# Performance work log

Hardware: AMD Instinct MI355X
Metric: run time of the kernel (lower is better)

Reference implementation:

```python
import jax, jax.numpy as jnp
import numpy as np

B, N, FEAT = 4, 100000, 11
NUM_SP = 512  # superpoints per sample
H1, H2, H3, E = 128, 256, 512, 384


def setup_inputs() -> dict:
    key = jax.random.key(0)
    ks = jax.random.split(key, 10)
    s = 0.02
    return {
        "full_features": jax.random.normal(ks[0], (B, N, FEAT), dtype=jnp.float32),
        "full_super_indices": jax.random.randint(ks[1], (B, N), 0, NUM_SP, dtype=jnp.int32),
        "W1": jax.random.normal(ks[2], (H1, FEAT), dtype=jnp.float32) * s,
        "b1": jnp.zeros((H1,), jnp.float32),
        "W2": jax.random.normal(ks[3], (H2, H1), dtype=jnp.float32) * s,
        "b2": jnp.zeros((H2,), jnp.float32),
        "W3": jax.random.normal(ks[4], (H3, H3), dtype=jnp.float32) * s,
        "b3": jnp.zeros((H3,), jnp.float32),
        "W4": jax.random.normal(ks[5], (E, H3), dtype=jnp.float32) * s,
        "b4": jnp.zeros((E,), jnp.float32),
    }


def reference(full_features, full_super_indices, W1, b1, W2, b2, W3, b3, W4, b4):
    # Vectorized form of the per-superpoint mini-PointNet:
    # conv1x1 MLP on points, segment-max pool, concat global+local, MLP, segment-max.
    x = full_features.reshape(B * N, FEAT)
    # first_conv: Conv1d(feat,128,1) -> Conv1d(128,256,1), no activation in between
    h = x @ W1.T + b1
    h = h @ W2.T + b2                                   # [B*N, 256]
    # global segment ids (batch-offset superpoint ids)
    seg = (full_super_indices.astype(jnp.int32) + jnp.arange(B, dtype=jnp.int32)[:, None] * NUM_SP).reshape(-1)
    gmax = jax.ops.segment_max(h, seg, num_segments=B * NUM_SP)  # [B*S, 256]
    g = gmax[seg]                                       # broadcast global feature back to points
    feat = jnp.concatenate([g, h], axis=-1)             # [B*N, 512] (global first, as in torch.cat)
    # second_conv: Conv1d(512,512,1) -> ReLU -> Conv1d(512,E,1)
    y = jax.nn.relu(feat @ W3.T + b3)
    y = y @ W4.T + b4                                   # [B*N, E]
    out = jax.ops.segment_max(y, seg, num_segments=B * NUM_SP)
    return out.reshape(B, NUM_SP, E)
```

## Files before the change

kernel.cpp:

```cpp
#include <hip/hip_runtime.h>
#include <hip/hip_bf16.h>
#include <math.h>

#define BB    4
#define NN    100000
#define NFEAT 11
#define NSP   512
#define NSEG  (BB*NSP)
#define NPTS  (BB*NN)
#define H2    256
#define H3    512
#define EE    384
#define MT    64
#define GS    (MT*8)
#define MI_N  (MT/16)
#define MAXL  15
#define RSEG  512
#define MAXS  12
#define ENCNI 0x007FFFFFu

typedef __attribute__((ext_vector_type(8))) short short8;
typedef __attribute__((ext_vector_type(4))) float f32x4;

__device__ __forceinline__ ushort f2bf(float f) {
  unsigned u = __builtin_bit_cast(unsigned, f);
  unsigned r = (u + 0x7FFFu + ((u >> 16) & 1u)) >> 16;
  return (ushort)r;
}
__device__ __forceinline__ unsigned encf(float f) {
  unsigned u = __builtin_bit_cast(unsigned, f);
  return u ^ ((unsigned)((int)u >> 31) | 0x80000000u);
}
__device__ __forceinline__ float decf(unsigned e) {
  unsigned u = (e & 0x80000000u) ? (e ^ 0x80000000u) : ~e;
  return __builtin_bit_cast(float, u);
}

__global__ void init_all(int* __restrict__ counts, int* __restrict__ cursor,
                         unsigned* __restrict__ gmaxEnc, unsigned* __restrict__ out_enc) {
  int i = blockIdx.x * 256 + threadIdx.x;
  if (i < NSEG * EE) out_enc[i] = ENCNI;
  if (i < NSEG * H2) gmaxEnc[i] = ENCNI;
  if (i < NSEG) { counts[i] = 0; cursor[i] = 0; }
}

__global__ void hist_kernel(const int* __restrict__ sidx, int* __restrict__ counts) {
  int i = blockIdx.x * blockDim.x + threadIdx.x;
  if (i < NPTS) {
    int seg = sidx[i] + (i / NN) * NSP;
    atomicAdd(&counts[seg], 1);
  }
}

__global__ void scan_kernel(const int* __restrict__ counts, int* __restrict__ offs) {
  __shared__ int buf[1024];
  int t = threadIdx.x;
  int c0 = counts[2 * t], c1 = counts[2 * t + 1];
  int s = c0 + c1;
  buf[t] = s;
  __syncthreads();
  for (int d = 1; d < 1024; d <<= 1) {
    int add = (t >= d) ? buf[t - d] : 0;
    __syncthreads();
    buf[t] += add;
    __syncthreads();
  }
  int incl = buf[t];
  int excl = incl - s;
  offs[2 * t] = excl;
  offs[2 * t + 1] = excl + c0;
  if (t == 1023) offs[2048] = incl;
}

__global__ void scatter_kernel(const int* __restrict__ sidx, const int* __restrict__ offs,
                               int* __restrict__ cursor, int* __restrict__ perm,
                               int* __restrict__ segp) {
  int i = blockIdx.x * blockDim.x + threadIdx.x;
  if (i < NPTS) {
    int seg = sidx[i] + (i / NN) * NSP;
    int pos = offs[seg] + atomicAdd(&cursor[seg], 1);
    perm[pos] = i;
    segp[pos] = seg;
  }
}

__global__ void prep_weights(const float* __restrict__ W1, const float* __restrict__ b1,
                             const float* __restrict__ W2, const float* __restrict__ b2,
                             const float* __restrict__ W3, const float* __restrict__ W4,
                             float* __restrict__ W12, float* __restrict__ b12,
                             float* __restrict__ W3gT, ushort* __restrict__ W3hP,
                             ushort* __restrict__ W4P) {
  int u = blockIdx.x * blockDim.x + threadIdx.x;
  if (u < H2 * NFEAT) {
    int c = u / NFEAT, f = u - c * NFEAT;
    float acc = 0.f;
    for (int j = 0; j < 128; ++j) acc += W2[c * 128 + j] * W1[j * NFEAT + f];
    W12[u] = acc;
  } else if (u < 3072) {
    int c = u - H2 * NFEAT;
    float acc = b2[c];
    for (int j = 0; j < 128; ++j) acc += W2[c * 128 + j] * b1[j];
    b12[c] = acc;
  } else if (u < 3072 + 131072) {
    int v = u - 3072;
    int c = v >> 9, o = v & 511;
    W3gT[v] = W3[o * H3 + c];
  } else if (u < 134144 + 16384) {
    int v = u - 134144;
    int ks = v >> 11, rem = v & 2047;
    int nt = rem >> 6, l = rem & 63;
    int n = nt * 16 + (l & 15);
    #pragma unroll
    for (int j = 0; j < 8; ++j) {
      int k = ks * 32 + (l >> 4) * 8 + j;
      W3hP[(size_t)v * 8 + j] = f2bf(W3[n * H3 + H2 + k]);
    }
  } else if (u < 150528 + 24576) {
    int v = u - 150528;
    int ks = v / 1536, rem = v - ks * 1536;
    int nt = rem >> 6, l = rem & 63;
    int n = nt * 16 + (l & 15);
    #pragma unroll
    for (int j = 0; j < 8; ++j) {
      int k = ks * 32 + (l >> 4) * 8 + j;
      W4P[(size_t)v * 8 + j] = f2bf(W4[n * H3 + k]);
    }
  }
}

template <bool STOREH>
__global__ __launch_bounds__(512) void gmax_kernel(
    const float* __restrict__ x, const int* __restrict__ perm,
    const int* __restrict__ segp,
    const float* __restrict__ W12, const float* __restrict__ b12,
    unsigned* __restrict__ gmaxEnc, ushort* __restrict__ hG) {
  __shared__ float xs[RSEG * NFEAT];
  __shared__ float W12s[H2 * NFEAT];
  __shared__ float b12s[H2];
  __shared__ int   segd[RSEG];
  __shared__ unsigned gmaxL[MAXS * H2];

  const int t = threadIdx.x;
  const int mbeg = blockIdx.x * RSEG;
  const int nvalid = min(RSEG, NPTS - mbeg);

  for (int u = t; u < RSEG * NFEAT; u += 512) {
    int p = u / NFEAT, f = u - p * NFEAT;
    xs[u] = (p < nvalid) ? x[(size_t)perm[mbeg + p] * NFEAT + f] : 0.f;
  }
  for (int u = t; u < H2 * NFEAT; u += 512) W12s[u] = W12[u];
  if (t < H2) b12s[t] = b12[t];
  segd[t] = (t < nvalid) ? segp[mbeg + t] : segp[mbeg + nvalid - 1];
  for (int u = t; u < MAXS * H2; u += 512) gmaxL[u] = ENCNI;
  __syncthreads();

  const int s_lo = segd[0];
  const int s_hi = segd[nvalid - 1];
  const bool fb = (s_hi - s_lo + 1) > MAXS;

  const int g  = t >> 4;
  const int r0 = t & 15;
  const int cb = g * 8;

  float w12r[8][NFEAT], bbr[8];
  #pragma unroll
  for (int cj = 0; cj < 8; ++cj) {
    bbr[cj] = b12s[cb + cj];
    #pragma unroll
    for (int f = 0; f < NFEAT; ++f) w12r[cj][f] = W12s[(cb + cj) * NFEAT + f];
  }

  float m[8];
  #pragma unroll
  for (int cj = 0; cj < 8; ++cj) m[cj] = -INFINITY;
  int cur = segd[r0];
  bool any = false;

  for (int k = 0; k < 32; ++k) {
    int row = r0 + k * 16;
    if (row >= nvalid) break;
    int sg = segd[row];
    if (sg != cur) {
      #pragma unroll
      for (int cj = 0; cj < 8; ++cj) {
        unsigned e = encf(m[cj]);
        if (fb) atomicMax(&gmaxEnc[(size_t)cur * H2 + cb + cj], e);
        else    atomicMax(&gmaxL[(cur - s_lo) * H2 + cb + cj], e);
      }
      cur = sg;
      #pragma unroll
      for (int cj = 0; cj < 8; ++cj) m[cj] = -INFINITY;
    }
    float acc[8];
    #pragma unroll
    for (int cj = 0; cj < 8; ++cj) acc[cj] = bbr[cj];
    #pragma unroll
    for (int f = 0; f < NFEAT; ++f) {
      float xv = xs[row * NFEAT + f];
      #pragma unroll
      for (int cj = 0; cj < 8; ++cj) acc[cj] += w12r[cj][f] * xv;
    }
    if (STOREH) {
      uint4 pkt;
      pkt.x = (unsigned)f2bf(acc[0]) | ((unsigned)f2bf(acc[1]) << 16);
      pkt.y = (unsigned)f2bf(acc[2]) | ((unsigned)f2bf(acc[3]) << 16);
      pkt.z = (unsigned)f2bf(acc[4]) | ((unsigned)f2bf(acc[5]) << 16);
      pkt.w = (unsigned)f2bf(acc[6]) | ((unsigned)f2bf(acc[7]) << 16);
      int pt = mbeg + row;
      *(uint4*)&hG[(size_t)(pt >> 6) * 16384 + ((size_t)g * 64 + (pt & 63)) * 8] = pkt;
    }
    #pragma unroll
    for (int cj = 0; cj < 8; ++cj) m[cj] = fmaxf(m[cj], acc[cj]);
    any = true;
  }
  if (any) {
    #pragma unroll
    for (int cj = 0; cj < 8; ++cj) {
      unsigned e = encf(m[cj]);
      if (fb) atomicMax(&gmaxEnc[(size_t)cur * H2 + cb + cj], e);
      else    atomicMax(&gmaxL[(cur - s_lo) * H2 + cb + cj], e);
    }
  }

  __syncthreads();
  if (!fb) {
    int nloc = s_hi - s_lo + 1;
    for (int u = t; u < nloc * H2; u += 512) {
      int sg = s_lo + (u >> 8);
      unsigned v = gmaxL[u];
      if (sg > s_lo && sg < s_hi) gmaxEnc[(size_t)sg * H2 + (u & 255)] = v;
      else atomicMax(&gmaxEnc[(size_t)sg * H2 + (u & 255)], v);
    }
  }
}

__global__ __launch_bounds__(256) void gpart_kernel(
    const unsigned* __restrict__ gmaxEnc, const float* __restrict__ W3gT,
    const float* __restrict__ b3, float* __restrict__ gpartG) {
  __shared__ float gm[8 * 256];
  const int t = threadIdx.x;
  const int b = blockIdx.x;
  for (int u = t; u < 8 * 256; u += 256) gm[u] = decf(gmaxEnc[(size_t)b * 8 * 256 + u]);
  __syncthreads();
  const float bb0 = b3[t], bb1 = b3[t + 256];
  float a0[8], a1[8];
  #pragma unroll
  for (int sg = 0; sg < 8; ++sg) { a0[sg] = bb0; a1[sg] = bb1; }
  for (int c = 0; c < 256; ++c) {
    float w0 = W3gT[c * 512 + t], w1 = W3gT[c * 512 + t + 256];
    #pragma unroll
    for (int sg = 0; sg < 8; ++sg) {
      float gv = gm[sg * 256 + c];
      a0[sg] += w0 * gv; a1[sg] += w1 * gv;
    }
  }
  #pragma unroll
  for (int sg = 0; sg < 8; ++sg) {
    size_t s = (size_t)b * 8 + sg;
    gpartG[s * 512 + t] = a0[sg];
    gpartG[s * 512 + t + 256] = a1[sg];
  }
}

__global__ void finalize_kernel(const unsigned* __restrict__ enc, float* __restrict__ out) {
  int i = blockIdx.x * 256 + threadIdx.x;
  if (i < NSEG * EE) out[i] = decf(enc[i]);
}

__global__ __launch_bounds__(512, 4) void main_v2(
    const int* __restrict__ segp, const ushort* __restrict__ hG,
    const ushort* __restrict__ W3hP, const ushort* __restrict__ W4P,
    const float* __restrict__ gpartG, const float* __restrict__ b4,
    unsigned* __restrict__ out_enc) {
  __shared__ __align__(16) ushort hsE[MT * 256];
  __shared__ __align__(16) ushort regB[MT * 256];
  __shared__ float gpartL[MAXL * 256];
  __shared__ int segdL[MT];
  __shared__ int s_loS, nlocS;

  const int t = threadIdx.x;
  const int w = t >> 6;
  const int l = t & 63;
  const int mbeg = blockIdx.x * MT;

  ushort* y1E = regB;
  unsigned* obuf = (unsigned*)regB;

  {
    const size_t tb = (size_t)blockIdx.x * (MT * 256);
    #pragma unroll
    for (int i = 0; i < 4; ++i)
      *(uint4*)&hsE[(size_t)(i * 512 + t) * 8] = *(const uint4*)&hG[tb + (size_t)(i * 512 + t) * 8];
  }
  if (t < MT) segdL[t] = segp[mbeg + t];
  __syncthreads();
  if (t == 0) {
    s_loS = segdL[0];
    nlocS = segdL[MT - 1] - segdL[0] + 1;
  }
  __syncthreads();
  const int s_lo = s_loS;
  const int nloc = nlocS;
  const bool fb = (nloc > MAXL);

  float b4v[3];
  #pragma unroll
  for (int ni = 0; ni < 3; ++ni) b4v[ni] = b4[w * 48 + ni * 16 + (l & 15)];

  f32x4 acc4[MI_N][3];
  #pragma unroll
  for (int mi = 0; mi < MI_N; ++mi)
    #pragma unroll
    for (int ni = 0; ni < 3; ++ni)
      acc4[mi][ni] = (f32x4){0.f, 0.f, 0.f, 0.f};

  #pragma unroll
  for (int hf = 0; hf < 2; ++hf) {
    if (!fb) {
      for (int u = t; u < nloc * 256; u += 512) {
        int sg = u >> 8, c = u & 255;
        gpartL[u] = gpartG[(size_t)(s_lo + sg) * 512 + hf * 256 + c];
      }
    }

    f32x4 acc3[MI_N][2];
    #pragma unroll
    for (int mi = 0; mi < MI_N; ++mi)
      #pragma unroll
      for (int ni = 0; ni < 2; ++ni)
        acc3[mi][ni] = (f32x4){0.f, 0.f, 0.f, 0.f};

    {
      short8 bcur[2][2], bnxt[2][2];
      #pragma unroll
      for (int c2 = 0; c2 < 2; ++c2)
        #pragma unroll
        for (int ni = 0; ni < 2; ++ni)
          bcur[c2][ni] = *(const short8*)&W3hP[(size_t)(((c2) * 32 + hf * 16 + w * 2 + ni) * 64 + l) * 8];
      #pragma unroll
      for (int kc = 0; kc < 4; ++kc) {
        if (kc < 3) {
          #pragma unroll
          for (int c2 = 0; c2 < 2; ++c2)
            #pragma unroll
            for (int ni = 0; ni < 2; ++ni)
              bnxt[c2][ni] = *(const short8*)&W3hP[(size_t)(((kc * 2 + 2 + c2) * 32 + hf * 16 + w * 2 + ni) * 64 + l) * 8];
        }
        #pragma unroll
        for (int c2 = 0; c2 < 2; ++c2) {
          const int ks = kc * 2 + c2;
          #pragma unroll
          for (int mi = 0; mi < MI_N; ++mi) {
            short8 a = *(const short8*)&hsE[(ks * 4 + (l >> 4)) * GS + (mi * 16 + (l & 15)) * 8];
            acc3[mi][0] = __builtin_amdgcn_mfma_f32_16x16x32_bf16(a, bcur[c2][0], acc3[mi][0], 0, 0, 0);
            acc3[mi][1] = __builtin_amdgcn_mfma_f32_16x16x32_bf16(a, bcur[c2][1], acc3[mi][1], 0, 0, 0);
          }
        }
        if (kc < 3) {
          #pragma unroll
          for (int c2 = 0; c2 < 2; ++c2)
            #pragma unroll
            for (int ni = 0; ni < 2; ++ni)
              bcur[c2][ni] = bnxt[c2][ni];
        }
      }
    }
    __syncthreads();

    #pragma unroll
    for (int mi = 0; mi < MI_N; ++mi)
      #pragma unroll
      for (int ni = 0; ni < 2; ++ni) {
        int colh = w * 32 + ni * 16 + (l & 15);
        #pragma unroll
        for (int r = 0; r < 4; ++r) {
          int row = mi * 16 + (l >> 4) * 4 + r;
          int sg = segdL[row];
          float bias = fb ? gpartG[(size_t)sg * 512 + hf * 256 + colh]
                          : gpartL[(sg - s_lo) * 256 + colh];
          float v = fmaxf(acc3[mi][ni][r] + bias, 0.f);
          y1E[(colh >> 3) * GS + row * 8 + (colh & 7)] = f2bf(v);
        }
      }
    __syncthreads();

    {
      short8 bcur[2][3], bnxt[2][3];
      #pragma unroll
      for (int c2 = 0; c2 < 2; ++c2)
        #pragma unroll
        for (int ni = 0; ni < 3; ++ni)
          bcur[c2][ni] = *(const short8*)&W4P[(size_t)(((hf * 8 + c2) * 24 + w * 3 + ni) * 64 + l) * 8];
      #pragma unroll
      for (int kc = 0; kc < 4; ++kc) {
        if (kc < 3) {
          #pragma unroll
          for (int c2 = 0; c2 < 2; ++c2)
            #pragma unroll
            for (int ni = 0; ni < 3; ++ni)
              bnxt[c2][ni] = *(const short8*)&W4P[(size_t)(((hf * 8 + kc * 2 + 2 + c2) * 24 + w * 3 + ni) * 64 + l) * 8];
        }
        #pragma unroll
        for (int c2 = 0; c2 < 2; ++c2) {
          const int ks = kc * 2 + c2;
          #pragma unroll
          for (int mi = 0; mi < MI_N; ++mi) {
            short8 a = *(const short8*)&y1E[(ks * 4 + (l >> 4)) * GS + (mi * 16 + (l & 15)) * 8];
            acc4[mi][0] = __builtin_amdgcn_mfma_f32_16x16x32_bf16(a, bcur[c2][0], acc4[mi][0], 0, 0, 0);
            acc4[mi][1] = __builtin_amdgcn_mfma_f32_16x16x32_bf16(a, bcur[c2][1], acc4[mi][1], 0, 0, 0);
            acc4[mi][2] = __builtin_amdgcn_mfma_f32_16x16x32_bf16(a, bcur[c2][2], acc4[mi][2], 0, 0, 0);
          }
        }
        if (kc < 3) {
          #pragma unroll
          for (int c2 = 0; c2 < 2; ++c2)
            #pragma unroll
            for (int ni = 0; ni < 3; ++ni)
              bcur[c2][ni] = bnxt[c2][ni];
        }
      }
    }
    __syncthreads();
  }

  if (!fb) {
    for (int u = t; u < nloc * EE; u += 512) obuf[u] = ENCNI;
    __syncthreads();
    #pragma unroll
    for (int mi = 0; mi < MI_N; ++mi) {
      int rbase = mi * 16 + (l >> 4) * 4;
      int sg0 = segdL[rbase], sg3 = segdL[rbase + 3];
      #pragma unroll
      for (int ni = 0; ni < 3; ++ni) {
        int col = w * 48 + ni * 16 + (l & 15);
        if (sg0 == sg3) {
          float m4 = fmaxf(fmaxf(acc4[mi][ni][0], acc4[mi][ni][1]),
                           fmaxf(acc4[mi][ni][2], acc4[mi][ni][3]));
          atomicMax(&obuf[(sg0 - s_lo) * EE + col], encf(m4 + b4v[ni]));
        } else {
          #pragma unroll
          for (int r = 0; r < 4; ++r)
            atomicMax(&obuf[(segdL[rbase + r] - s_lo) * EE + col],
                      encf(acc4[mi][ni][r] + b4v[ni]));
        }
      }
    }
    __syncthreads();
    for (int u = t; u < nloc * EE; u += 512) {
      unsigned e = obuf[u];
      if (e != ENCNI)
        atomicMax(&out_enc[(size_t)(s_lo + u / EE) * EE + (u % EE)], e);
    }
  } else {
    #pragma unroll
    for (int mi = 0; mi < MI_N; ++mi)
      #pragma unroll
      for (int ni = 0; ni < 3; ++ni) {
        int col = w * 48 + ni * 16 + (l & 15);
        #pragma unroll
        for (int r = 0; r < 4; ++r) {
          int row = mi * 16 + (l >> 4) * 4 + r;
          unsigned e = encf(acc4[mi][ni][r] + b4v[ni]);
          atomicMax(&out_enc[(size_t)segdL[row] * EE + col], e);
        }
      }
  }
}

__global__ __launch_bounds__(512, 4) void main_kernel(
    const float* __restrict__ x, const int* __restrict__ perm,
    const int* __restrict__ segp,
    const float* __restrict__ W12, const float* __restrict__ b12,
    const ushort* __restrict__ W3hP, const ushort* __restrict__ W4P,
    const float* __restrict__ gpartG, const float* __restrict__ b4,
    unsigned* __restrict__ out_enc) {
  __shared__ __align__(16) ushort hsE[MT * 256];
  __shared__ __align__(16) ushort regB[MT * 256];
  __shared__ float gpartL[MAXL * 256];
  __shared__ int segdL[MT];
  __shared__ int s_loS, nlocS;

  const int t = threadIdx.x;
  const int w = t >> 6;
  const int l = t & 63;
  const int mbeg = blockIdx.x * MT;
  const int nvalid = min(MT, NPTS - mbeg);

  float* xsF  = (float*)regB;
  float* W12s = xsF + 704;
  float* b12s = W12s + 2816;
  ushort* y1E = regB;
  unsigned* obuf = (unsigned*)regB;

  for (int u = t; u < MT * NFEAT; u += 512) {
    int p = u / NFEAT, f = u - p * NFEAT;
    xsF[u] = (p < nvalid) ? x[(size_t)perm[mbeg + p] * NFEAT + f] : 0.f;
  }
  for (int u = t; u < 2816; u += 512) W12s[u] = W12[u];
  if (t < 256) b12s[t] = b12[t];
  if (t < MT) segdL[t] = (t < nvalid) ? segp[mbeg + t] : 0;
  __syncthreads();
  if (t == 0) {
    s_loS = segdL[0];
    nlocS = segdL[nvalid - 1] - segdL[0] + 1;
  }
  __syncthreads();
  const int s_lo = s_loS;
  const int nloc = nlocS;
  const bool fb = (nloc > MAXL);
  if (t < MT && t >= nvalid) segdL[t] = s_lo;

  #pragma unroll
  for (int i = 0; i < 4; ++i) {
    int gran = i * 8 + w;
    int cb = gran * 8;
    int row = l;
    uint4 pkt = {0, 0, 0, 0};
    if (row < nvalid) {
      float acc[8];
      #pragma unroll
      for (int cj = 0; cj < 8; ++cj) acc[cj] = b12s[cb + cj];
      #pragma unroll
      for (int f = 0; f < NFEAT; ++f) {
        float xv = xsF[row * NFEAT + f];
        #pragma unroll
        for (int cj = 0; cj < 8; ++cj) acc[cj] += W12s[(cb + cj) * NFEAT + f] * xv;
      }
      pkt.x = (unsigned)f2bf(acc[0]) | ((unsigned)f2bf(acc[1]) << 16);
      pkt.y = (unsigned)f2bf(acc[2]) | ((unsigned)f2bf(acc[3]) << 16);
      pkt.z = (unsigned)f2bf(acc[4]) | ((unsigned)f2bf(acc[5]) << 16);
      pkt.w = (unsigned)f2bf(acc[6]) | ((unsigned)f2bf(acc[7]) << 16);
    }
    *(uint4*)&hsE[gran * GS + row * 8] = pkt;
  }
  __syncthreads();

  float b4v[3];
  #pragma unroll
  for (int ni = 0; ni < 3; ++ni) b4v[ni] = b4[w * 48 + ni * 16 + (l & 15)];

  f32x4 acc4[MI_N][3];
  #pragma unroll
  for (int mi = 0; mi < MI_N; ++mi)
    #pragma unroll
    for (int ni = 0; ni < 3; ++ni)
      acc4[mi][ni] = (f32x4){0.f, 0.f, 0.f, 0.f};

  #pragma unroll
  for (int hf = 0; hf < 2; ++hf) {
    if (!fb) {
      for (int u = t; u < nloc * 256; u += 512) {
        int sg = u >> 8, c = u & 255;
        gpartL[u] = gpartG[(size_t)(s_lo + sg) * 512 + hf * 256 + c];
      }
    }

    f32x4 acc3[MI_N][2];
    #pragma unroll
    for (int mi = 0; mi < MI_N; ++mi)
      #pragma unroll
      for (int ni = 0; ni < 2; ++ni)
        acc3[mi][ni] = (f32x4){0.f, 0.f, 0.f, 0.f};

    {
      short8 bcur[2][2], bnxt[2][2];
      #pragma unroll
      for (int c2 = 0; c2 < 2; ++c2)
        #pragma unroll
        for (int ni = 0; ni < 2; ++ni)
          bcur[c2][ni] = *(const short8*)&W3hP[(size_t)(((c2) * 32 + hf * 16 + w * 2 + ni) * 64 + l) * 8];
      #pragma unroll
      for (int kc = 0; kc < 4; ++kc) {
        if (kc < 3) {
          #pragma unroll
          for (int c2 = 0; c2 < 2; ++c2)
            #pragma unroll
            for (int ni = 0; ni < 2; ++ni)
              bnxt[c2][ni] = *(const short8*)&W3hP[(size_t)(((kc * 2 + 2 + c2) * 32 + hf * 16 + w * 2 + ni) * 64 + l) * 8];
        }
        #pragma unroll
        for (int c2 = 0; c2 < 2; ++c2) {
          const int ks = kc * 2 + c2;
          #pragma unroll
          for (int mi = 0; mi < MI_N; ++mi) {
            short8 a = *(const short8*)&hsE[(ks * 4 + (l >> 4)) * GS + (mi * 16 + (l & 15)) * 8];
            acc3[mi][0] = __builtin_amdgcn_mfma_f32_16x16x32_bf16(a, bcur[c2][0], acc3[mi][0], 0, 0, 0);
            acc3[mi][1] = __builtin_amdgcn_mfma_f32_16x16x32_bf16(a, bcur[c2][1], acc3[mi][1], 0, 0, 0);
          }
        }
        if (kc < 3) {
          #pragma unroll
          for (int c2 = 0; c2 < 2; ++c2)
            #pragma unroll
            for (int ni = 0; ni < 2; ++ni)
              bcur[c2][ni] = bnxt[c2][ni];
        }
      }
    }
    __syncthreads();

    #pragma unroll
    for (int mi = 0; mi < MI_N; ++mi)
      #pragma unroll
      for (int ni = 0; ni < 2; ++ni) {
        int colh = w * 32 + ni * 16 + (l & 15);
        #pragma unroll
        for (int r = 0; r < 4; ++r) {
          int row = mi * 16 + (l >> 4) * 4 + r;
          int sg = segdL[row];
          float bias = fb ? gpartG[(size_t)sg * 512 + hf * 256 + colh]
                          : gpartL[(sg - s_lo) * 256 + colh];
          float v = fmaxf(acc3[mi][ni][r] + bias, 0.f);
          y1E[(colh >> 3) * GS + row * 8 + (colh & 7)] = f2bf(v);
        }
      }
    __syncthreads();

    {
      short8 bcur[2][3], bnxt[2][3];
      #pragma unroll
      for (int c2 = 0; c2 < 2; ++c2)
        #pragma unroll
        for (int ni = 0; ni < 3; ++ni)
          bcur[c2][ni] = *(const short8*)&W4P[(size_t)(((hf * 8 + c2) * 24 + w * 3 + ni) * 64 + l) * 8];
      #pragma unroll
      for (int kc = 0; kc < 4; ++kc) {
        if (kc < 3) {
          #pragma unroll
          for (int c2 = 0; c2 < 2; ++c2)
            #pragma unroll
            for (int ni = 0; ni < 3; ++ni)
              bnxt[c2][ni] = *(const short8*)&W4P[(size_t)(((hf * 8 + kc * 2 + 2 + c2) * 24 + w * 3 + ni) * 64 + l) * 8];
        }
        #pragma unroll
        for (int c2 = 0; c2 < 2; ++c2) {
          const int ks = kc * 2 + c2;
          #pragma unroll
          for (int mi = 0; mi < MI_N; ++mi) {
            short8 a = *(const short8*)&y1E[(ks * 4 + (l >> 4)) * GS + (mi * 16 + (l & 15)) * 8];
            acc4[mi][0] = __builtin_amdgcn_mfma_f32_16x16x32_bf16(a, bcur[c2][0], acc4[mi][0], 0, 0, 0);
            acc4[mi][1] = __builtin_amdgcn_mfma_f32_16x16x32_bf16(a, bcur[c2][1], acc4[mi][1], 0, 0, 0);
            acc4[mi][2] = __builtin_amdgcn_mfma_f32_16x16x32_bf16(a, bcur[c2][2], acc4[mi][2], 0, 0, 0);
          }
        }
        if (kc < 3) {
          #pragma unroll
          for (int c2 = 0; c2 < 2; ++c2)
            #pragma unroll
            for (int ni = 0; ni < 3; ++ni)
              bcur[c2][ni] = bnxt[c2][ni];
        }
      }
    }
    __syncthreads();
  }

  if (!fb) {
    for (int u = t; u < nloc * EE; u += 512) obuf[u] = ENCNI;
    __syncthreads();
    #pragma unroll
    for (int mi = 0; mi < MI_N; ++mi)
      #pragma unroll
      for (int ni = 0; ni < 3; ++ni) {
        int col = w * 48 + ni * 16 + (l & 15);
        #pragma unroll
        for (int r = 0; r < 4; ++r) {
          int row = mi * 16 + (l >> 4) * 4 + r;
          if (row < nvalid) {
            unsigned e = encf(acc4[mi][ni][r] + b4v[ni]);
            atomicMax(&obuf[(segdL[row] - s_lo) * EE + col], e);
          }
        }
      }
    __syncthreads();
    for (int u = t; u < nloc * EE; u += 512) {
      unsigned e = obuf[u];
      if (e != ENCNI)
        atomicMax(&out_enc[(size_t)(s_lo + u / EE) * EE + (u % EE)], e);
    }
  } else {
    #pragma unroll
    for (int mi = 0; mi < MI_N; ++mi)
      #pragma unroll
      for (int ni = 0; ni < 3; ++ni) {
        int col = w * 48 + ni * 16 + (l & 15);
        #pragma unroll
        for (int r = 0; r < 4; ++r) {
          int row = mi * 16 + (l >> 4) * 4 + r;
          if (row < nvalid) {
            unsigned e = encf(acc4[mi][ni][r] + b4v[ni]);
            atomicMax(&out_enc[(size_t)segdL[row] * EE + col], e);
          }
        }
      }
  }
}

extern "C" void kernel_launch(void* const* d_in, const int* in_sizes, int n_in,
                              void* d_out, int out_size, void* d_ws, size_t ws_size,
                              hipStream_t stream) {
  (void)in_sizes; (void)n_in; (void)out_size;
  const float* x    = (const float*)d_in[0];
  const int*   sidx = (const int*)d_in[1];
  const float* W1   = (const float*)d_in[2];
  const float* b1   = (const float*)d_in[3];
  const float* W2   = (const float*)d_in[4];
  const float* b2   = (const float*)d_in[5];
  const float* W3   = (const float*)d_in[6];
  const float* b3   = (const float*)d_in[7];
  const float* W4   = (const float*)d_in[8];
  const float* b4   = (const float*)d_in[9];
  float* out = (float*)d_out;

  char* ws = (char*)d_ws;
  size_t off = 0;
  auto alloc = [&](size_t bytes) {
    void* p = ws + off;
    off = (off + bytes + 255) & ~(size_t)255;
    return p;
  };
  int*      counts  = (int*)alloc(NSEG * 4);
  int*      cursor  = (int*)alloc(NSEG * 4);
  int*      offs    = (int*)alloc((NSEG + 1) * 4);
  int*      perm    = (int*)alloc((size_t)NPTS * 4);
  int*      segp    = (int*)alloc((size_t)NPTS * 4);
  float*    W12     = (float*)alloc(H2 * NFEAT * 4);
  float*    b12     = (float*)alloc(H2 * 4);
  float*    W3gT    = (float*)alloc((size_t)H2 * H3 * 4);
  ushort*   W3hP    = (ushort*)alloc((size_t)131072 * 2);
  ushort*   W4P     = (ushort*)alloc((size_t)196608 * 2);
  unsigned* gmaxEnc = (unsigned*)alloc((size_t)NSEG * H2 * 4);
  float*    gpartG  = (float*)alloc((size_t)NSEG * H3 * 4);
  unsigned* out_enc = (unsigned*)alloc((size_t)NSEG * EE * 4);
  ushort*   hG      = (ushort*)alloc((size_t)NPTS * 256 * 2);
  const bool useH = (off <= ws_size);

  init_all<<<(NSEG * EE + 255) / 256, 256, 0, stream>>>(counts, cursor, gmaxEnc, out_enc);
  const int preptotal = 150528 + 24576;
  prep_weights<<<(preptotal + 255) / 256, 256, 0, stream>>>(W1, b1, W2, b2, W3, W4,
                                                            W12, b12, W3gT, W3hP, W4P);
  hist_kernel<<<(NPTS + 255) / 256, 256, 0, stream>>>(sidx, counts);
  scan_kernel<<<1, 1024, 0, stream>>>(counts, offs);
  scatter_kernel<<<(NPTS + 255) / 256, 256, 0, stream>>>(sidx, offs, cursor, perm, segp);
  if (useH) {
    gmax_kernel<true><<<(NPTS + RSEG - 1) / RSEG, 512, 0, stream>>>(x, perm, segp, W12, b12, gmaxEnc, hG);
    gpart_kernel<<<NSEG / 8, 256, 0, stream>>>(gmaxEnc, W3gT, b3, gpartG);
    main_v2<<<NPTS / MT, 512, 0, stream>>>(segp, hG, W3hP, W4P, gpartG, b4, out_enc);
  } else {
    gmax_kernel<false><<<(NPTS + RSEG - 1) / RSEG, 512, 0, stream>>>(x, perm, segp, W12, b12, gmaxEnc, hG);
    gpart_kernel<<<NSEG / 8, 256, 0, stream>>>(gmaxEnc, W3gT, b3, gpartG);
    main_kernel<<<NPTS / MT, 512, 0, stream>>>(x, perm, segp, W12, b12,
                                               W3hP, W4P, gpartG, b4, out_enc);
  }
  finalize_kernel<<<(NSEG * EE + 255) / 256, 256, 0, stream>>>(out_enc, out);
}
```

Baseline: 650.8 us.

## Interleave W3 second-half and W4 first-half MFMAs, merge init into prep

Merges the init kernel into the weight-prep kernel to save a launch. In the main kernel, the two-half loop is restructured so the second W3 half-GEMM runs in the same k-loop as the first W4 half-GEMM, giving more independent MFMA chains to hide latency. Explicit double-buffered weight prefetch is replaced with simple per-step loads, and s_setprio raises wave priority around the MFMA loops. This raises register pressure by keeping acc3 and acc4 live together and relies on the compiler to schedule the global loads.

```diff
diff --git a/kernel.cpp b/kernel.cpp
--- a/kernel.cpp
+++ b/kernel.cpp
@@ -36,61 +36,19 @@
   return __builtin_bit_cast(float, u);
 }
 
-__global__ void init_all(int* __restrict__ counts, int* __restrict__ cursor,
-                         unsigned* __restrict__ gmaxEnc, unsigned* __restrict__ out_enc) {
-  int i = blockIdx.x * 256 + threadIdx.x;
-  if (i < NSEG * EE) out_enc[i] = ENCNI;
-  if (i < NSEG * H2) gmaxEnc[i] = ENCNI;
-  if (i < NSEG) { counts[i] = 0; cursor[i] = 0; }
-}
-
-__global__ void hist_kernel(const int* __restrict__ sidx, int* __restrict__ counts) {
-  int i = blockIdx.x * blockDim.x + threadIdx.x;
-  if (i < NPTS) {
-    int seg = sidx[i] + (i / NN) * NSP;
-    atomicAdd(&counts[seg], 1);
-  }
-}
-
-__global__ void scan_kernel(const int* __restrict__ counts, int* __restrict__ offs) {
-  __shared__ int buf[1024];
-  int t = threadIdx.x;
-  int c0 = counts[2 * t], c1 = counts[2 * t + 1];
-  int s = c0 + c1;
-  buf[t] = s;
-  __syncthreads();
-  for (int d = 1; d < 1024; d <<= 1) {
-    int add = (t >= d) ? buf[t - d] : 0;
-    __syncthreads();
-    buf[t] += add;
-    __syncthreads();
-  }
-  int incl = buf[t];
-  int excl = incl - s;
-  offs[2 * t] = excl;
-  offs[2 * t + 1] = excl + c0;
-  if (t == 1023) offs[2048] = incl;
-}
-
-__global__ void scatter_kernel(const int* __restrict__ sidx, const int* __restrict__ offs,
-                               int* __restrict__ cursor, int* __restrict__ perm,
-                               int* __restrict__ segp) {
-  int i = blockIdx.x * blockDim.x + threadIdx.x;
-  if (i < NPTS) {
-    int seg = sidx[i] + (i / NN) * NSP;
-    int pos = offs[seg] + atomicAdd(&cursor[seg], 1);
-    perm[pos] = i;
-    segp[pos] = seg;
-  }
-}
-
-__global__ void prep_weights(const float* __restrict__ W1, const float* __restrict__ b1,
-                             const float* __restrict__ W2, const float* __restrict__ b2,
-                             const float* __restrict__ W3, const float* __restrict__ W4,
-                             float* __restrict__ W12, float* __restrict__ b12,
-                             float* __restrict__ W3gT, ushort* __restrict__ W3hP,
-                             ushort* __restrict__ W4P) {
-  int u = blockIdx.x * blockDim.x + threadIdx.x;
+__global__ void prep_init(const float* __restrict__ W1, const float* __restrict__ b1,
+                          const float* __restrict__ W2, const float* __restrict__ b2,
+                          const float* __restrict__ W3, const float* __restrict__ W4,
+                          float* __restrict__ W12, float* __restrict__ b12,
+                          float* __restrict__ W3gT, ushort* __restrict__ W3hP,
+                          ushort* __restrict__ W4P,
+                          int* __restrict__ counts, int* __restrict__ cursor,
+                          unsigned* __restrict__ gmaxEnc, unsigned* __restrict__ out_enc) {
+  int u = blockIdx.x * 256 + threadIdx.x;
+  if (u < NSEG * EE) out_enc[u] = ENCNI;
+  if (u < NSEG * H2) gmaxEnc[u] = ENCNI;
+  if (u < NSEG) { counts[u] = 0; cursor[u] = 0; }
+
   if (u < H2 * NFEAT) {
     int c = u / NFEAT, f = u - c * NFEAT;
     float acc = 0.f;
@@ -128,6 +86,46 @@
   }
 }
 
+__global__ void hist_kernel(const int* __restrict__ sidx, int* __restrict__ counts) {
+  int i = blockIdx.x * blockDim.x + threadIdx.x;
+  if (i < NPTS) {
+    int seg = sidx[i] + (i / NN) * NSP;
+    atomicAdd(&counts[seg], 1);
+  }
+}
+
+__global__ void scan_kernel(const int* __restrict__ counts, int* __restrict__ offs) {
+  __shared__ int buf[1024];
+  int t = threadIdx.x;
+  int c0 = counts[2 * t], c1 = counts[2 * t + 1];
+  int s = c0 + c1;
+  buf[t] = s;
+  __syncthreads();
+  for (int d = 1; d < 1024; d <<= 1) {
+    int add = (t >= d) ? buf[t - d] : 0;
+    __syncthreads();
+    buf[t] += add;
+    __syncthreads();
+  }
+  int incl = buf[t];
+  int excl = incl - s;
+  offs[2 * t] = excl;
+  offs[2 * t + 1] = excl + c0;
+  if (t == 1023) offs[2048] = incl;
+}
+
+__global__ void scatter_kernel(const int* __restrict__ sidx, const int* __restrict__ offs,
+                               int* __restrict__ cursor, int* __restrict__ perm,
+                               int* __restrict__ segp) {
+  int i = blockIdx.x * blockDim.x + threadIdx.x;
+  if (i < NPTS) {
+    int seg = sidx[i] + (i / NN) * NSP;
+    int pos = offs[seg] + atomicAdd(&cursor[seg], 1);
+    perm[pos] = i;
+    segp[pos] = seg;
+  }
+}
+
 template <bool STOREH>
 __global__ __launch_bounds__(512) void gmax_kernel(
     const float* __restrict__ x, const int* __restrict__ perm,
@@ -267,7 +265,7 @@
   if (i < NSEG * EE) out[i] = decf(enc[i]);
 }
 
-__global__ __launch_bounds__(512, 4) void main_v2(
+__global__ __launch_bounds__(512, 4) void main_v3(
     const int* __restrict__ segp, const ushort* __restrict__ hG,
     const ushort* __restrict__ W3hP, const ushort* __restrict__ W4P,
     const float* __restrict__ gpartG, const float* __restrict__ b4,
@@ -314,114 +312,122 @@
     for (int ni = 0; ni < 3; ++ni)
       acc4[mi][ni] = (f32x4){0.f, 0.f, 0.f, 0.f};
 
-  #pragma unroll
-  for (int hf = 0; hf < 2; ++hf) {
-    if (!fb) {
-      for (int u = t; u < nloc * 256; u += 512) {
-        int sg = u >> 8, c = u & 255;
-        gpartL[u] = gpartG[(size_t)(s_lo + sg) * 512 + hf * 256 + c];
-      }
-    }
-
-    f32x4 acc3[MI_N][2];
-    #pragma unroll
-    for (int mi = 0; mi < MI_N; ++mi)
-      #pragma unroll
-      for (int ni = 0; ni < 2; ++ni)
-        acc3[mi][ni] = (f32x4){0.f, 0.f, 0.f, 0.f};
-
+  f32x4 acc3[MI_N][2];
+
+  if (!fb) {
+    for (int u = t; u < nloc * 256; u += 512)
+      gpartL[u] = gpartG[(size_t)(s_lo + (u >> 8)) * 512 + (u & 255)];
+  }
+
+  #pragma unroll
+  for (int mi = 0; mi < MI_N; ++mi) {
+    acc3[mi][0] = (f32x4){0.f, 0.f, 0.f, 0.f};
+    acc3[mi][1] = (f32x4){0.f, 0.f, 0.f, 0.f};
+  }
+  __builtin_amdgcn_s_setprio(1);
+  #pragma unroll
+  for (int ks = 0; ks < 8; ++ks) {
+    short8 b0 = *(const short8*)&W3hP[(size_t)((ks * 32 + w * 2 + 0) * 64 + l) * 8];
+    short8 b1 = *(const short8*)&W3hP[(size_t)((ks * 32 + w * 2 + 1) * 64 + l) * 8];
+    #pragma unroll
+    for (int mi = 0; mi < MI_N; ++mi) {
+      short8 a = *(const short8*)&hsE[(ks * 4 + (l >> 4)) * GS + (mi * 16 + (l & 15)) * 8];
+      acc3[mi][0] = __builtin_amdgcn_mfma_f32_16x16x32_bf16(a, b0, acc3[mi][0], 0, 0, 0);
+      acc3[mi][1] = __builtin_amdgcn_mfma_f32_16x16x32_bf16(a, b1, acc3[mi][1], 0, 0, 0);
+    }
+  }
+  __builtin_amdgcn_s_setprio(0);
+  __syncthreads();
+
+  #pragma unroll
+  for (int mi = 0; mi < MI_N; ++mi)
+    #pragma unroll
+    for (int ni = 0; ni < 2; ++ni) {
+      int colh = w * 32 + ni * 16 + (l & 15);
+      #pragma unroll
+      for (int r = 0; r < 4; ++r) {
+        int row = mi * 16 + (l >> 4) * 4 + r;
+        int sg = segdL[row];
+        float bias = fb ? gpartG[(size_t)sg * 512 + colh]
+                        : gpartL[(sg - s_lo) * 256 + colh];
+        float v = fmaxf(acc3[mi][ni][r] + bias, 0.f);
+        y1E[(colh >> 3) * GS + row * 8 + (colh & 7)] = f2bf(v);
+      }
+    }
+  __syncthreads();
+
+  if (!fb) {
+    for (int u = t; u < nloc * 256; u += 512)
+      gpartL[u] = gpartG[(size_t)(s_lo + (u >> 8)) * 512 + 256 + (u & 255)];
+  }
+
+  #pragma unroll
+  for (int mi = 0; mi < MI_N; ++mi) {
+    acc3[mi][0] = (f32x4){0.f, 0.f, 0.f, 0.f};
+    acc3[mi][1] = (f32x4){0.f, 0.f, 0.f, 0.f};
+  }
+  __builtin_amdgcn_s_setprio(1);
+  #pragma unroll
+  for (int ks = 0; ks < 8; ++ks) {
     {
-      short8 bcur[2][2], bnxt[2][2];
-      #pragma unroll
-      for (int c2 = 0; c2 < 2; ++c2)
-        #pragma unroll
-        for (int ni = 0; ni < 2; ++ni)
-          bcur[c2][ni] = *(const short8*)&W3hP[(size_t)(((c2) * 32 + hf * 16 + w * 2 + ni) * 64 + l) * 8];
-      #pragma unroll
-      for (int kc = 0; kc < 4; ++kc) {
-        if (kc < 3) {
-          #pragma unroll
-          for (int c2 = 0; c2 < 2; ++c2)
-            #pragma unroll
-            for (int ni = 0; ni < 2; ++ni)
-              bnxt[c2][ni] = *(const short8*)&W3hP[(size_t)(((kc * 2 + 2 + c2) * 32 + hf * 16 + w * 2 + ni) * 64 + l) * 8];
-        }
-        #pragma unroll
-        for (int c2 = 0; c2 < 2; ++c2) {
-          const int ks = kc * 2 + c2;
-          #pragma unroll
-          for (int mi = 0; mi < MI_N; ++mi) {
-            short8 a = *(const short8*)&hsE[(ks * 4 + (l >> 4)) * GS + (mi * 16 + (l & 15)) * 8];
-            acc3[mi][0] = __builtin_amdgcn_mfma_f32_16x16x32_bf16(a, bcur[c2][0], acc3[mi][0], 0, 0, 0);
-            acc3[mi][1] = __builtin_amdgcn_mfma_f32_16x16x32_bf16(a, bcur[c2][1], acc3[mi][1], 0, 0, 0);
-          }
-        }
-        if (kc < 3) {
-          #pragma unroll
-          for (int c2 = 0; c2 < 2; ++c2)
-            #pragma unroll
-            for (int ni = 0; ni < 2; ++ni)
-              bcur[c2][ni] = bnxt[c2][ni];
-        }
-      }
-    }
-    __syncthreads();
-
-    #pragma unroll
-    for (int mi = 0; mi < MI_N; ++mi)
-      #pragma unroll
-      for (int ni = 0; ni < 2; ++ni) {
-        int colh = w * 32 + ni * 16 + (l & 15);
-        #pragma unroll
-        for (int r = 0; r < 4; ++r) {
-          int row = mi * 16 + (l >> 4) * 4 + r;
-          int sg = segdL[row];
-          float bias = fb ? gpartG[(size_t)sg * 512 + hf * 256 + colh]
-                          : gpartL[(sg - s_lo) * 256 + colh];
-          float v = fmaxf(acc3[mi][ni][r] + bias, 0.f);
-          y1E[(colh >> 3) * GS + row * 8 + (colh & 7)] = f2bf(v);
-        }
-      }
-    __syncthreads();
-
+      short8 b0 = *(const short8*)&W3hP[(size_t)((ks * 32 + 16 + w * 2 + 0) * 64 + l) * 8];
+      short8 b1 = *(const short8*)&W3hP[(size_t)((ks * 32 + 16 + w * 2 + 1) * 64 + l) * 8];
+      #pragma unroll
+      for (int mi = 0; mi < MI_N; ++mi) {
+        short8 a = *(const short8*)&hsE[(ks * 4 + (l >> 4)) * GS + (mi * 16 + (l & 15)) * 8];
+        acc3[mi][0] = __builtin_amdgcn_mfma_f32_16x16x32_bf16(a, b0, acc3[mi][0], 0, 0, 0);
+        acc3[mi][1] = __builtin_amdgcn_mfma_f32_16x16x32_bf16(a, b1, acc3[mi][1], 0, 0, 0);
+      }
+    }
     {
-      short8 bcur[2][3], bnxt[2][3];
-      #pragma unroll
-      for (int c2 = 0; c2 < 2; ++c2)
-        #pragma unroll
-        for (int ni = 0; ni < 3; ++ni)
-          bcur[c2][ni] = *(const short8*)&W4P[(size_t)(((hf * 8 + c2) * 24 + w * 3 + ni) * 64 + l) * 8];
-      #pragma unroll
-      for (int kc = 0; kc < 4; ++kc) {
-        if (kc < 3) {
-          #pragma unroll
-          for (int c2 = 0; c2 < 2; ++c2)
-            #pragma unroll
-            for (int ni = 0; ni < 3; ++ni)
-              bnxt[c2][ni] = *(const short8*)&W4P[(size_t)(((hf * 8 + kc * 2 + 2 + c2) * 24 + w * 3 + ni) * 64 + l) * 8];
-        }
-        #pragma unroll
-        for (int c2 = 0; c2 < 2; ++c2) {
-          const int ks = kc * 2 + c2;
-          #pragma unroll
-          for (int mi = 0; mi < MI_N; ++mi) {
-            short8 a = *(const short8*)&y1E[(ks * 4 + (l >> 4)) * GS + (mi * 16 + (l & 15)) * 8];
-            acc4[mi][0] = __builtin_amdgcn_mfma_f32_16x16x32_bf16(a, bcur[c2][0], acc4[mi][0], 0, 0, 0);
-            acc4[mi][1] = __builtin_amdgcn_mfma_f32_16x16x32_bf16(a, bcur[c2][1], acc4[mi][1], 0, 0, 0);
-            acc4[mi][2] = __builtin_amdgcn_mfma_f32_16x16x32_bf16(a, bcur[c2][2], acc4[mi][2], 0, 0, 0);
-          }
-        }
-        if (kc < 3) {
-          #pragma unroll
-          for (int c2 = 0; c2 < 2; ++c2)
-            #pragma unroll
-            for (int ni = 0; ni < 3; ++ni)
-              bcur[c2][ni] = bnxt[c2][ni];
-        }
-      }
-    }
-    __syncthreads();
-  }
+      short8 d0 = *(const short8*)&W4P[(size_t)((ks * 24 + w * 3 + 0) * 64 + l) * 8];
+      short8 d1 = *(const short8*)&W4P[(size_t)((ks * 24 + w * 3 + 1) * 64 + l) * 8];
+      short8 d2 = *(const short8*)&W4P[(size_t)((ks * 24 + w * 3 + 2) * 64 + l) * 8];
+      #pragma unroll
+      for (int mi = 0; mi < MI_N; ++mi) {
+        short8 a = *(const short8*)&y1E[(ks * 4 + (l >> 4)) * GS + (mi * 16 + (l & 15)) * 8];
+        acc4[mi][0] = __builtin_amdgcn_mfma_f32_16x16x32_bf16(a, d0, acc4[mi][0], 0, 0, 0);
+        acc4[mi][1] = __builtin_amdgcn_mfma_f32_16x16x32_bf16(a, d1, acc4[mi][1], 0, 0, 0);
+        acc4[mi][2] = __builtin_amdgcn_mfma_f32_16x16x32_bf16(a, d2, acc4[mi][2], 0, 0, 0);
+      }
+    }
+  }
+  __builtin_amdgcn_s_setprio(0);
+  __syncthreads();
+
+  #pragma unroll
+  for (int mi = 0; mi < MI_N; ++mi)
+    #pragma unroll
+    for (int ni = 0; ni < 2; ++ni) {
+      int colh = w * 32 + ni * 16 + (l & 15);
+      #pragma unroll
+      for (int r = 0; r < 4; ++r) {
+        int row = mi * 16 + (l >> 4) * 4 + r;
+        int sg = segdL[row];
+        float bias = fb ? gpartG[(size_t)sg * 512 + 256 + colh]
+                        : gpartL[(sg - s_lo) * 256 + colh];
+        float v = fmaxf(acc3[mi][ni][r] + bias, 0.f);
+        y1E[(colh >> 3) * GS + row * 8 + (colh & 7)] = f2bf(v);
+      }
+    }
+  __syncthreads();
+
+  __builtin_amdgcn_s_setprio(1);
+  #pragma unroll
+  for (int ks = 0; ks < 8; ++ks) {
+    short8 d0 = *(const short8*)&W4P[(size_t)(((8 + ks) * 24 + w * 3 + 0) * 64 + l) * 8];
+    short8 d1 = *(const short8*)&W4P[(size_t)(((8 + ks) * 24 + w * 3 + 1) * 64 + l) * 8];
+    short8 d2 = *(const short8*)&W4P[(size_t)(((8 + ks) * 24 + w * 3 + 2) * 64 + l) * 8];
+    #pragma unroll
+    for (int mi = 0; mi < MI_N; ++mi) {
+      short8 a = *(const short8*)&y1E[(ks * 4 + (l >> 4)) * GS + (mi * 16 + (l & 15)) * 8];
+      acc4[mi][0] = __builtin_amdgcn_mfma_f32_16x16x32_bf16(a, d0, acc4[mi][0], 0, 0, 0);
+      acc4[mi][1] = __builtin_amdgcn_mfma_f32_16x16x32_bf16(a, d1, acc4[mi][1], 0, 0, 0);
+      acc4[mi][2] = __builtin_amdgcn_mfma_f32_16x16x32_bf16(a, d2, acc4[mi][2], 0, 0, 0);
+    }
+  }
+  __builtin_amdgcn_s_setprio(0);
+  __syncthreads();
 
   if (!fb) {
     for (int u = t; u < nloc * EE; u += 512) obuf[u] = ENCNI;
@@ -562,39 +568,15 @@
       for (int ni = 0; ni < 2; ++ni)
         acc3[mi][ni] = (f32x4){0.f, 0.f, 0.f, 0.f};
 
-    {
-      short8 bcur[2][2], bnxt[2][2];
-      #pragma unroll
-      for (int c2 = 0; c2 < 2; ++c2)
-        #pragma unroll
-        for (int ni = 0; ni < 2; ++ni)
-          bcur[c2][ni] = *(const short8*)&W3hP[(size_t)(((c2) * 32 + hf * 16 + w * 2 + ni) * 64 + l) * 8];
-      #pragma unroll
-      for (int kc = 0; kc < 4; ++kc) {
-        if (kc < 3) {
-          #pragma unroll
-          for (int c2 = 0; c2 < 2; ++c2)
-            #pragma unroll
-            for (int ni = 0; ni < 2; ++ni)
-              bnxt[c2][ni] = *(const short8*)&W3hP[(size_t)(((kc * 2 + 2 + c2) * 32 + hf * 16 + w * 2 + ni) * 64 + l) * 8];
-        }
-        #pragma unroll
-        for (int c2 = 0; c2 < 2; ++c2) {
-          const int ks = kc * 2 + c2;
-          #pragma unroll
-          for (int mi = 0; mi < MI_N; ++mi) {
-            short8 a = *(const short8*)&hsE[(ks * 4 + (l >> 4)) * GS + (mi * 16 + (l & 15)) * 8];
-            acc3[mi][0] = __builtin_amdgcn_mfma_f32_16x16x32_bf16(a, bcur[c2][0], acc3[mi][0], 0, 0, 0);
-            acc3[mi][1] = __builtin_amdgcn_mfma_f32_16x16x32_bf16(a, bcur[c2][1], acc3[mi][1], 0, 0, 0);
-          }
-        }
-        if (kc < 3) {
-          #pragma unroll
-          for (int c2 = 0; c2 < 2; ++c2)
-            #pragma unroll
-            for (int ni = 0; ni < 2; ++ni)
-              bcur[c2][ni] = bnxt[c2][ni];
-        }
+    #pragma unroll
+    for (int ks = 0; ks < 8; ++ks) {
+      short8 b0 = *(const short8*)&W3hP[(size_t)((ks * 32 + hf * 16 + w * 2 + 0) * 64 + l) * 8];
+      short8 b1 = *(const short8*)&W3hP[(size_t)((ks * 32 + hf * 16 + w * 2 + 1) * 64 + l) * 8];
+      #pragma unroll
+      for (int mi = 0; mi < MI_N; ++mi) {
+        short8 a = *(const short8*)&hsE[(ks * 4 + (l >> 4)) * GS + (mi * 16 + (l & 15)) * 8];
+        acc3[mi][0] = __builtin_amdgcn_mfma_f32_16x16x32_bf16(a, b0, acc3[mi][0], 0, 0, 0);
+        acc3[mi][1] = __builtin_amdgcn_mfma_f32_16x16x32_bf16(a, b1, acc3[mi][1], 0, 0, 0);
       }
     }
     __syncthreads();
@@ -616,40 +598,17 @@
       }
     __syncthreads();
 
-    {
-      short8 bcur[2][3], bnxt[2][3];
-      #pragma unroll
-      for (int c2 = 0; c2 < 2; ++c2)
-        #pragma unroll
-        for (int ni = 0; ni < 3; ++ni)
-          bcur[c2][ni] = *(const short8*)&W4P[(size_t)(((hf * 8 + c2) * 24 + w * 3 + ni) * 64 + l) * 8];
-      #pragma unroll
-      for (int kc = 0; kc < 4; ++kc) {
-        if (kc < 3) {
-          #pragma unroll
-          for (int c2 = 0; c2 < 2; ++c2)
-            #pragma unroll
-            for (int ni = 0; ni < 3; ++ni)
-              bnxt[c2][ni] = *(const short8*)&W4P[(size_t)(((hf * 8 + kc * 2 + 2 + c2) * 24 + w * 3 + ni) * 64 + l) * 8];
-        }
-        #pragma unroll
-        for (int c2 = 0; c2 < 2; ++c2) {
-          const int ks = kc * 2 + c2;
-          #pragma unroll
-          for (int mi = 0; mi < MI_N; ++mi) {
-            short8 a = *(const short8*)&y1E[(ks * 4 + (l >> 4)) * GS + (mi * 16 + (l & 15)) * 8];
-            acc4[mi][0] = __builtin_amdgcn_mfma_f32_16x16x32_bf16(a, bcur[c2][0], acc4[mi][0], 0, 0, 0);
-            acc4[mi][1] = __builtin_amdgcn_mfma_f32_16x16x32_bf16(a, bcur[c2][1], acc4[mi][1], 0, 0, 0);
-            acc4[mi][2] = __builtin_amdgcn_mfma_f32_16x16x32_bf16(a, bcur[c2][2], acc4[mi][2], 0, 0, 0);
-          }
-        }
-        if (kc < 3) {
-          #pragma unroll
-          for (int c2 = 0; c2 < 2; ++c2)
-            #pragma unroll
-            for (int ni = 0; ni < 3; ++ni)
-              bcur[c2][ni] = bnxt[c2][ni];
-        }
+    #pragma unroll
+    for (int ks = 0; ks < 8; ++ks) {
+      short8 d0 = *(const short8*)&W4P[(size_t)(((hf * 8 + ks) * 24 + w * 3 + 0) * 64 + l) * 8];
+      short8 d1 = *(const short8*)&W4P[(size_t)(((hf * 8 + ks) * 24 + w * 3 + 1) * 64 + l) * 8];
+      short8 d2 = *(const short8*)&W4P[(size_t)(((hf * 8 + ks) * 24 + w * 3 + 2) * 64 + l) * 8];
+      #pragma unroll
+      for (int mi = 0; mi < MI_N; ++mi) {
+        short8 a = *(const short8*)&y1E[(ks * 4 + (l >> 4)) * GS + (mi * 16 + (l & 15)) * 8];
+        acc4[mi][0] = __builtin_amdgcn_mfma_f32_16x16x32_bf16(a, d0, acc4[mi][0], 0, 0, 0);
+        acc4[mi][1] = __builtin_amdgcn_mfma_f32_16x16x32_bf16(a, d1, acc4[mi][1], 0, 0, 0);
+        acc4[mi][2] = __builtin_amdgcn_mfma_f32_16x16x32_bf16(a, d2, acc4[mi][2], 0, 0, 0);
       }
     }
     __syncthreads();
@@ -735,17 +694,16 @@
   ushort*   hG      = (ushort*)alloc((size_t)NPTS * 256 * 2);
   const bool useH = (off <= ws_size);
 
-  init_all<<<(NSEG * EE + 255) / 256, 256, 0, stream>>>(counts, cursor, gmaxEnc, out_enc);
-  const int preptotal = 150528 + 24576;
-  prep_weights<<<(preptotal + 255) / 256, 256, 0, stream>>>(W1, b1, W2, b2, W3, W4,
-                                                            W12, b12, W3gT, W3hP, W4P);
+  prep_init<<<(NSEG * EE + 255) / 256, 256, 0, stream>>>(W1, b1, W2, b2, W3, W4,
+                                                         W12, b12, W3gT, W3hP, W4P,
+                                                         counts, cursor, gmaxEnc, out_enc);
   hist_kernel<<<(NPTS + 255) / 256, 256, 0, stream>>>(sidx, counts);
   scan_kernel<<<1, 1024, 0, stream>>>(counts, offs);
   scatter_kernel<<<(NPTS + 255) / 256, 256, 0, stream>>>(sidx, offs, cursor, perm, segp);
   if (useH) {
     gmax_kernel<true><<<(NPTS + RSEG - 1) / RSEG, 512, 0, stream>>>(x, perm, segp, W12, b12, gmaxEnc, hG);
     gpart_kernel<<<NSEG / 8, 256, 0, stream>>>(gmaxEnc, W3gT, b3, gpartG);
-    main_v2<<<NPTS / MT, 512, 0, stream>>>(segp, hG, W3hP, W4P, gpartG, b4, out_enc);
+    main_v3<<<NPTS / MT, 512, 0, stream>>>(segp, hG, W3hP, W4P, gpartG, b4, out_enc);
   } else {
     gmax_kernel<false><<<(NPTS + RSEG - 1) / RSEG, 512, 0, stream>>>(x, perm, segp, W12, b12, gmaxEnc, hG);
     gpart_kernel<<<NSEG / 8, 256, 0, stream>>>(gmaxEnc, W3gT, b3, gpartG);
```

New measurement: 761.2 us. 1.17x slower.
